# Optimization experiments

Hardware: AMD Instinct MI355X
Metric: run time of the kernel (lower is better)

## Reference

```python
import jax, jax.numpy as jnp
import numpy as np
import math

B, L, S, D = 4, 4096, 4096, 256
EPS = 1e-5

def _layernorm(x, g, b):
    mu = jnp.mean(x, axis=-1, keepdims=True)
    var = jnp.mean(jnp.square(x - mu), axis=-1, keepdims=True)
    return (x - mu) * jax.lax.rsqrt(var + EPS) * g + b

def setup_inputs() -> dict:
    key = jax.random.key(0)
    ks = jax.random.split(key, 14)
    s = 1.0 / math.sqrt(D)
    s2 = 1.0 / math.sqrt(2 * D)
    inp = {
        "source": jax.random.normal(ks[0], (B, L, D), jnp.float32),
        "target": jax.random.normal(ks[1], (B, S, D), jnp.float32),
        # linear weights stored as [in, out]
        "Wq": jax.random.uniform(ks[2], (D, D), jnp.float32, -s, s),
        "bq": jnp.zeros((D,), jnp.float32),
        "Wk": jax.random.uniform(ks[3], (D, D), jnp.float32, -s, s),
        "bk": jnp.zeros((D,), jnp.float32),
        "Wv": jax.random.uniform(ks[4], (D, D), jnp.float32, -s, s),
        "bv": jnp.zeros((D,), jnp.float32),
        "Wm": jax.random.uniform(ks[5], (D, D), jnp.float32, -s, s),
        "bm": jnp.zeros((D,), jnp.float32),
        "g1": jnp.ones((D,), jnp.float32),
        "beta1": jnp.zeros((D,), jnp.float32),
        "W1": jax.random.uniform(ks[6], (2 * D, 2 * D), jnp.float32, -s2, s2),
        "W2": jax.random.uniform(ks[7], (2 * D, D), jnp.float32, -s2, s2),
        "g2": jnp.ones((D,), jnp.float32),
        "beta2": jnp.zeros((D,), jnp.float32),
    }
    return inp

def reference(source, target, Wq, bq, Wk, bk, Wv, bv, Wm, bm, g1, beta1, W1, W2, g2, beta2):
    q = source @ Wq + bq              # [B, L, D]
    k = target @ Wk + bk              # [B, S, D]
    v = target @ Wv + bv              # [B, S, D]
    scale = 1.0 / math.sqrt(D)
    scores = jnp.einsum("bld,bsd->bls", q, k) * scale   # [B, L, S] materialized, as in source
    attn = jax.nn.softmax(scores, axis=-1)
    message = jnp.einsum("bls,bsd->bld", attn, v)        # [B, L, D]
    message = message @ Wm + bm
    message = _layernorm(message, g1, beta1)
    h = jnp.concatenate([source, message], axis=-1)      # [B, L, 2D]
    h = jax.nn.gelu(h @ W1, approximate=False)           # torch GELU is exact erf
    message = _layernorm(h @ W2, g2, beta2)
    return source + message
```

## Files before the change

### kernel.cpp

```cpp
#include <hip/hip_runtime.h>

typedef __bf16 bf16x8 __attribute__((ext_vector_type(8)));
typedef float f32x16 __attribute__((ext_vector_type(16)));
typedef float f32x4 __attribute__((ext_vector_type(4)));
typedef unsigned int u32;
typedef unsigned int u32x4 __attribute__((ext_vector_type(4)));
typedef unsigned short u16;
typedef unsigned short u16x4 __attribute__((ext_vector_type(4)));
typedef unsigned short u16x8 __attribute__((ext_vector_type(8)));

#define DEV static __device__ __forceinline__
#define AS1 __attribute__((address_space(1)))
#define AS3 __attribute__((address_space(3)))

DEV u16 f2bf(float f){
  unsigned u = __float_as_uint(f);
  u += 0x7FFFu + ((u >> 16) & 1u);
  return (u16)(u >> 16);
}
DEV float bf2f(u16 h){ return __uint_as_float(((u32)h) << 16); }

DEV void stage16(const u16* gsrc, const u16* ldst){
  __builtin_amdgcn_global_load_lds((const AS1 u32*)(unsigned long long)gsrc,
                                   (AS3 u32*)(u32)(unsigned long long)ldst,
                                   16, 0, 0);
}

constexpr int BATCH = 4, LQ = 4096, SK = 4096, DH = 256, BL = BATCH * LQ;
constexpr int NHALF = 2;
constexpr int ITERS = SK / NHALF / 64;

__global__ void prep_weights(const float* __restrict__ Wq, const float* __restrict__ Wk,
                             const float* __restrict__ Wv, const float* __restrict__ Wm,
                             const float* __restrict__ W1, const float* __restrict__ W2,
                             const float* __restrict__ bk, const float* __restrict__ bv,
                             u16* __restrict__ WqT, u16* __restrict__ WkvT,
                             u16* __restrict__ WmT,
                             u16* __restrict__ W1T, u16* __restrict__ W2T,
                             float* __restrict__ bkv){
  int idx = blockIdx.x * 256 + threadIdx.x;
  if (idx < 262144){
    int which = idx >> 16, i2 = idx & 65535;
    int r = i2 >> 8, c = i2 & 255;
    const float* S = (which==0)?Wq:(which==1)?Wk:(which==2)?Wv:Wm;
    u16*         D = (which==0)?WqT:(which==1)?WkvT:(which==2)?(WkvT+65536):WmT;
    D[c*256 + r] = f2bf(S[i2]);
  } else if (idx < 524288){
    int i2 = idx - 262144;
    int r = i2 >> 9, c = i2 & 511;
    W1T[c*512 + r] = f2bf(W1[i2]);
  } else if (idx < 655360){
    int i2 = idx - 524288;
    int r = i2 >> 8, c = i2 & 255;
    W2T[(size_t)c*512 + r] = f2bf(W2[i2]);
  } else if (idx < 655872){
    int i2 = idx - 655360;
    bkv[i2] = (i2 < 256) ? bk[i2] : bv[i2 - 256];
  }
}

template<bool A_F32, int EPI, bool WH>
__global__ __launch_bounds__(256, 2) void gemm128(
  const void* __restrict__ Ap, int lda, const u16* __restrict__ BTp,
  const float* __restrict__ bias, void* __restrict__ outp, void* __restrict__ outp2,
  u16* __restrict__ hcat,
  int M, int N, int K, float scale)
{
  __shared__ u16 A_lds[128 * 64];
  __shared__ u16 B_lds[128 * 64];
  const int tid = threadIdx.x, lane = tid & 63, wid = tid >> 6;
  const int ql = lane & 31, g = lane >> 5;
  const int m0 = blockIdx.y * 128, n0 = blockIdx.x * 128;
  const int mr = (wid & 1) * 64, nr = (wid >> 1) * 64;

  f32x16 acc[2][2] = {};
  f32x4 afreg[8];
  u32x4 abreg[4];
  u32x4 breg[4];
  const float* Af = (const float*)Ap;
  const u16*   Ab = (const u16*)Ap;

#define G_LOAD_A(kb) do { \
    if constexpr (A_F32){ \
      _Pragma("unroll") \
      for (int i = 0; i < 8; i++){ int item = tid + i*256; int r = item>>4, c = (item&15)*4; \
        afreg[i] = *(const f32x4*)&Af[(size_t)(m0+r)*lda + (kb)*64 + c]; } \
    } else { \
      _Pragma("unroll") \
      for (int i = 0; i < 4; i++){ int item = tid + i*256; int r = item>>3, c = (item&7)*8; \
        abreg[i] = *(const u32x4*)&Ab[(size_t)(m0+r)*lda + (kb)*64 + c]; } \
    } \
  } while(0)
#define G_LOAD_B(kb) do { \
    _Pragma("unroll") \
    for (int i = 0; i < 4; i++){ int item = tid + i*256; int r = item>>3, c = (item&7)*8; \
      breg[i] = *(const u32x4*)&BTp[(size_t)(n0+r)*K + (kb)*64 + c]; } \
  } while(0)

  G_LOAD_A(0); G_LOAD_B(0);

  const int nkb = K >> 6;
  for (int kb = 0; kb < nkb; ++kb){
    __syncthreads();
    if constexpr (A_F32){
      #pragma unroll
      for (int i = 0; i < 8; i++){ int item = tid + i*256; int r = item>>4, c = (item&15)*4;
        u16x4 h; h[0]=f2bf(afreg[i][0]); h[1]=f2bf(afreg[i][1]);
                 h[2]=f2bf(afreg[i][2]); h[3]=f2bf(afreg[i][3]);
        *(u16x4*)&A_lds[r*64 + (c ^ ((r&7)*8))] = h;
        if constexpr (WH){
          if (n0 == 0) *(u16x4*)&hcat[(size_t)(m0+r)*512 + kb*64 + c] = h;
        }
      }
    } else {
      #pragma unroll
      for (int i = 0; i < 4; i++){ int item = tid + i*256; int r = item>>3, c = (item&7)*8;
        *(u32x4*)&A_lds[r*64 + (c ^ ((r&7)*8))] = abreg[i]; }
    }
    #pragma unroll
    for (int i = 0; i < 4; i++){ int item = tid + i*256; int r = item>>3, c = (item&7)*8;
      *(u32x4*)&B_lds[r*64 + (c ^ ((r&7)*8))] = breg[i]; }
    __syncthreads();
    if (kb + 1 < nkb){ G_LOAD_A(kb+1); G_LOAD_B(kb+1); }

    #pragma unroll
    for (int kk = 0; kk < 4; kk++){
      bf16x8 af[2], bf[2];
      #pragma unroll
      for (int mi = 0; mi < 2; mi++)
        af[mi] = __builtin_bit_cast(bf16x8,
          *(const u32x4*)&A_lds[(mr+mi*32+ql)*64 + ((kk*16+g*8) ^ ((ql&7)*8))]);
      #pragma unroll
      for (int ni = 0; ni < 2; ni++)
        bf[ni] = __builtin_bit_cast(bf16x8,
          *(const u32x4*)&B_lds[(nr+ni*32+ql)*64 + ((kk*16+g*8) ^ ((ql&7)*8))]);
      #pragma unroll
      for (int mi = 0; mi < 2; mi++)
        #pragma unroll
        for (int ni = 0; ni < 2; ni++)
          acc[mi][ni] = __builtin_amdgcn_mfma_f32_32x32x16_bf16(af[mi], bf[ni], acc[mi][ni], 0, 0, 0);
    }
  }

  #pragma unroll
  for (int mi = 0; mi < 2; mi++){
    #pragma unroll
    for (int ni = 0; ni < 2; ni++){
      const int col = n0 + nr + ni*32 + ql;
      const float bv = bias ? bias[col] : 0.f;
      if constexpr (EPI == 4){
        if (col < 256){
          #pragma unroll
          for (int j = 0; j < 16; j++){
            int row = m0 + mr + mi*32 + (j&3) + 8*(j>>2) + 4*g;
            ((u16*)outp)[(size_t)row*256 + col] = f2bf(acc[mi][ni][j] + bv);
          }
        } else {
          const int col2 = col - 256;
          #pragma unroll
          for (int qd = 0; qd < 4; qd++){
            u16x4 h;
            #pragma unroll
            for (int i = 0; i < 4; i++) h[i] = f2bf(acc[mi][ni][qd*4+i] + bv);
            int row0 = m0 + mr + mi*32 + qd*8 + 4*g;
            int bb = row0 >> 12, ss = row0 & 4095;
            *(u16x4*)&((u16*)outp2)[((size_t)bb*DH + col2)*SK + ss] = h;
          }
        }
      } else {
        #pragma unroll
        for (int j = 0; j < 16; j++){
          int row = m0 + mr + mi*32 + (j&3) + 8*(j>>2) + 4*g;
          float v = acc[mi][ni][j] + bv;
          if constexpr (EPI == 0){
            ((u16*)outp)[(size_t)row*N + col] = f2bf(v * scale);
          } else {
            v = 0.5f * v * (1.f + erff(v * 0.70710678118f));
            ((u16*)outp)[(size_t)row*N + col] = f2bf(v);
          }
        }
      }
    }
  }
}

template<int MODE>
__global__ __launch_bounds__(256, 2) void gemm_ln(
  const u16* __restrict__ Ab, const u16* __restrict__ opart,
  const float* __restrict__ stats,
  const u16* __restrict__ BTp, const float* __restrict__ bias,
  const float* __restrict__ gamma, const float* __restrict__ beta,
  const float* __restrict__ src, void* __restrict__ outp, int K)
{
  __shared__ __align__(16) char smem[36864];
  u16* A_lds = (u16*)smem;
  u16* B_lds = (u16*)(smem + 4096);
  float* scratch = (float*)smem;

  const int tid = threadIdx.x, lane = tid & 63, wid = tid >> 6;
  const int ql = lane & 31, g = lane >> 5;
  const int m0 = blockIdx.x * 32;
  const int ar = tid >> 3, ac = (tid & 7) * 8;

  float winv = 0.f;
  if constexpr (MODE == 0){
    int row = m0 + ar;
    winv = 1.f / (stats[row] + stats[(size_t)BL + row]);
  }

  f32x16 acc[2] = {};
  u32x4 areg, areg2;
  u32x4 breg[8];

#define LN_LOAD_A(kb) do { \
    if constexpr (MODE == 0){ \
      areg  = *(const u32x4*)&opart[(size_t)(m0+ar)*DH + (kb)*64 + ac]; \
      areg2 = *(const u32x4*)&opart[(size_t)BL*DH + (size_t)(m0+ar)*DH + (kb)*64 + ac]; \
    } else { \
      areg  = *(const u32x4*)&Ab[(size_t)(m0+ar)*K + (kb)*64 + ac]; \
    } } while(0)
#define LN_LOAD_B(kb) do { \
    _Pragma("unroll") \
    for (int i = 0; i < 8; i++){ int item = tid + i*256; int r = item>>3, c = (item&7)*8; \
      breg[i] = *(const u32x4*)&BTp[(size_t)r*K + (kb)*64 + c]; } \
  } while(0)

  LN_LOAD_A(0); LN_LOAD_B(0);

  const int nkb = K >> 6;
  for (int kb = 0; kb < nkb; ++kb){
    __syncthreads();
    if constexpr (MODE == 0){
      u16x8 h;
      #pragma unroll
      for (int e = 0; e < 8; e++){
        u16 h0 = (u16)(areg[e>>1]  >> ((e&1)*16));
        u16 h1 = (u16)(areg2[e>>1] >> ((e&1)*16));
        h[e] = f2bf((bf2f(h0) + bf2f(h1)) * winv);
      }
      *(u16x8*)&A_lds[ar*64 + (ac ^ ((ar&7)*8))] = h;
    } else {
      *(u32x4*)&A_lds[ar*64 + (ac ^ ((ar&7)*8))] = areg;
    }
    #pragma unroll
    for (int i = 0; i < 8; i++){ int item = tid + i*256; int r = item>>3, c = (item&7)*8;
      *(u32x4*)&B_lds[r*64 + (c ^ ((r&7)*8))] = breg[i]; }
    __syncthreads();
    if (kb + 1 < nkb){ LN_LOAD_A(kb+1); LN_LOAD_B(kb+1); }

    #pragma unroll
    for (int kk = 0; kk < 4; kk++){
      bf16x8 af = __builtin_bit_cast(bf16x8,
        *(const u32x4*)&A_lds[ql*64 + ((kk*16+g*8) ^ ((ql&7)*8))]);
      #pragma unroll
      for (int ni = 0; ni < 2; ni++){
        bf16x8 bf = __builtin_bit_cast(bf16x8,
          *(const u32x4*)&B_lds[(wid*64+ni*32+ql)*64 + ((kk*16+g*8) ^ ((ql&7)*8))]);
        acc[ni] = __builtin_amdgcn_mfma_f32_32x32x16_bf16(af, bf, acc[ni], 0, 0, 0);
      }
    }
  }

  __syncthreads();

  float bv0 = 0.f, bv1 = 0.f;
  if constexpr (MODE == 0){ bv0 = bias[wid*64 + ql]; bv1 = bias[wid*64 + 32 + ql]; }
  #pragma unroll
  for (int ni = 0; ni < 2; ni++)
    #pragma unroll
    for (int j = 0; j < 16; j++){
      int row = (j&3) + 8*(j>>2) + 4*g;
      scratch[row*257 + wid*64 + ni*32 + ql] = acc[ni][j] + (ni ? bv1 : bv0);
    }
  __syncthreads();

  f32x4 gv = *(const f32x4*)&gamma[lane*4];
  f32x4 bvv = *(const f32x4*)&beta[lane*4];
  #pragma unroll
  for (int rr = 0; rr < 8; rr++){
    const int row = wid*8 + rr;
    f32x4 v = *(const f32x4*)&scratch[row*257 + lane*4];
    float s1 = v[0]+v[1]+v[2]+v[3];
    float s2 = v[0]*v[0]+v[1]*v[1]+v[2]*v[2]+v[3]*v[3];
    #pragma unroll
    for (int m = 1; m < 64; m <<= 1){ s1 += __shfl_xor(s1, m, 64); s2 += __shfl_xor(s2, m, 64); }
    float mu = s1 * (1.f/DH);
    float var = s2 * (1.f/DH) - mu*mu;
    float rstd = rsqrtf(var + 1e-5f);
    if constexpr (MODE == 0){
      u16x4 h;
      #pragma unroll
      for (int i = 0; i < 4; i++) h[i] = f2bf((v[i]-mu)*rstd*gv[i] + bvv[i]);
      *(u16x4*)&((u16*)outp)[(size_t)(m0+row)*512 + 256 + lane*4] = h;
    } else {
      f32x4 s = *(const f32x4*)&src[(size_t)(m0+row)*DH + lane*4];
      f32x4 o;
      #pragma unroll
      for (int i = 0; i < 4; i++) o[i] = s[i] + (v[i]-mu)*rstd*gv[i] + bvv[i];
      *(f32x4*)&((float*)outp)[(size_t)(m0+row)*DH + lane*4] = o;
    }
  }
}

__global__ __launch_bounds__(512, 2) void attn_kernel(
  const u16* __restrict__ qb, const u16* __restrict__ kb,
  const u16* __restrict__ vtb, u16* __restrict__ opart, float* __restrict__ stats)
{
  __shared__ u16 K_lds[2][64 * 256];
  __shared__ u16 VT_lds[2][256 * 64];
  __shared__ u32x4 P_exch[4][4][64];
  __shared__ float L_exch[4][2][32];

  const int tid = threadIdx.x;
  const int wid = tid >> 6, lane = tid & 63;
  const int ql = lane & 31, g = lane >> 5;
  const int qpair = wid >> 1, sh = wid & 1;
  const int b = blockIdx.y, half = blockIdx.z;
  const int qrow0 = blockIdx.x * 128 + qpair * 32;
  const int s0base = half * (SK / NHALF);

  const u16* kbase = kb  + (size_t)b * SK * DH;
  const u16* vbase = vtb + (size_t)b * DH * SK;

#define STAGE_K(bi, s0) do { \
    _Pragma("unroll") \
    for (int i = 0; i < 4; i++){ \
      int grp = tid + i*512; int s = grp>>5, slot = grp&31; \
      stage16(kbase + (size_t)((s0)+s)*DH + ((slot ^ (s&31))<<3), \
              &K_lds[bi][(i*512 + wid*64)*8]); \
    } } while(0)
#define STAGE_V(bi, s0) do { \
    _Pragma("unroll") \
    for (int i = 0; i < 4; i++){ \
      int grp = tid + i*512; int d = grp>>3, slot = grp&7; \
      stage16(vbase + (size_t)d*SK + (s0) + ((slot ^ (d&7))<<3), \
              &VT_lds[bi][(i*512 + wid*64)*8]); \
    } } while(0)

  STAGE_K(0, s0base);
  STAGE_V(0, s0base);

  bf16x8 qf[16];
  {
    const u16* qp = qb + ((size_t)(b*LQ + qrow0 + ql)) * DH + g * 8;
    #pragma unroll
    for (int kk = 0; kk < 16; kk++)
      qf[kk] = __builtin_bit_cast(bf16x8, *(const u32x4*)(qp + kk*16));
  }

  f32x16 accO[4] = {};
  float l_lane = 0.f;

  __syncthreads();

  for (int it = 0; it < ITERS; ++it){
    const int cur = it & 1;
    if (it + 1 < ITERS){
      STAGE_K(cur ^ 1, s0base + (it+1)*64);
      STAGE_V(cur ^ 1, s0base + (it+1)*64);
    }

    f32x16 ps = {};
    __builtin_amdgcn_s_setprio(1);
    #pragma unroll
    for (int kk = 0; kk < 16; ++kk){
      bf16x8 kf = __builtin_bit_cast(bf16x8,
        *(const u32x4*)&K_lds[cur][(sh*32+ql)*256 + (((kk*2+g) ^ ql)<<3)]);
      ps = __builtin_amdgcn_mfma_f32_32x32x16_bf16(kf, qf[kk], ps, 0, 0, 0);
    }
    __builtin_amdgcn_s_setprio(0);

    #pragma unroll
    for (int j = 0; j < 16; j++) ps[j] = exp2f(ps[j]);
    float s8[8];
    #pragma unroll
    for (int j = 0; j < 8; j++) s8[j] = ps[j] + ps[j+8];
    l_lane += ((s8[0]+s8[4]) + (s8[1]+s8[5])) + ((s8[2]+s8[6]) + (s8[3]+s8[7]));

    u32 Wp[4][2];
    #pragma unroll
    for (int qd = 0; qd < 4; qd++)
      #pragma unroll
      for (int h = 0; h < 2; h++){
        float lo = ps[qd*4 + 2*h], hi = ps[qd*4 + 2*h + 1];
        asm("v_cvt_pk_bf16_f32 %0, %1, %2" : "=v"(Wp[qd][h]) : "v"(lo), "v"(hi));
      }
    #pragma unroll
    for (int i = 0; i < 2; i++){
      const int qp2 = i * 2;
      u32 a0 = Wp[qp2][0], b0 = Wp[qp2+1][0];
      u32 a1 = Wp[qp2][1], b1 = Wp[qp2+1][1];
      asm("v_permlane32_swap_b32 %0, %1" : "+v"(a0), "+v"(b0));
      asm("v_permlane32_swap_b32 %0, %1" : "+v"(a1), "+v"(b1));
      u32x4 w; w[0] = a0; w[1] = a1; w[2] = b0; w[3] = b1;
      P_exch[qpair][sh*2 + i][lane] = w;
    }

    asm volatile("s_waitcnt lgkmcnt(0)" ::: "memory");
    __builtin_amdgcn_s_barrier();
    __builtin_amdgcn_sched_barrier(0);

    bf16x8 pf0 = __builtin_bit_cast(bf16x8, P_exch[qpair][0][lane]);
    bf16x8 pf1 = __builtin_bit_cast(bf16x8, P_exch[qpair][1][lane]);
    bf16x8 pf2 = __builtin_bit_cast(bf16x8, P_exch[qpair][2][lane]);
    bf16x8 pf3 = __builtin_bit_cast(bf16x8, P_exch[qpair][3][lane]);

    __builtin_amdgcn_s_setprio(1);
    #pragma unroll
    for (int dt = 0; dt < 4; dt++){
      const int dtg = sh*4 + dt;
      bf16x8 vf0 = __builtin_bit_cast(bf16x8,
        *(const u32x4*)&VT_lds[cur][(dtg*32+ql)*64 + (((0*2+g) ^ (ql&7))<<3)]);
      accO[dt] = __builtin_amdgcn_mfma_f32_32x32x16_bf16(vf0, pf0, accO[dt], 0, 0, 0);
      bf16x8 vf1 = __builtin_bit_cast(bf16x8,
        *(const u32x4*)&VT_lds[cur][(dtg*32+ql)*64 + (((1*2+g) ^ (ql&7))<<3)]);
      accO[dt] = __builtin_amdgcn_mfma_f32_32x32x16_bf16(vf1, pf1, accO[dt], 0, 0, 0);
      bf16x8 vf2 = __builtin_bit_cast(bf16x8,
        *(const u32x4*)&VT_lds[cur][(dtg*32+ql)*64 + (((2*2+g) ^ (ql&7))<<3)]);
      accO[dt] = __builtin_amdgcn_mfma_f32_32x32x16_bf16(vf2, pf2, accO[dt], 0, 0, 0);
      bf16x8 vf3 = __builtin_bit_cast(bf16x8,
        *(const u32x4*)&VT_lds[cur][(dtg*32+ql)*64 + (((3*2+g) ^ (ql&7))<<3)]);
      accO[dt] = __builtin_amdgcn_mfma_f32_32x32x16_bf16(vf3, pf3, accO[dt], 0, 0, 0);
    }
    __builtin_amdgcn_s_setprio(0);

    asm volatile("s_waitcnt vmcnt(0) lgkmcnt(0)" ::: "memory");
    __builtin_amdgcn_s_barrier();
    __builtin_amdgcn_sched_barrier(0);
  }

  float l_run = l_lane + __shfl_xor(l_lane, 32, 64);
  if (g == 0) L_exch[qpair][sh][ql] = l_run;
  __syncthreads();
  float l_tot = l_run + L_exch[qpair][sh^1][ql];

  const int rowb = b * LQ + qrow0;
  if (sh == 0 && g == 0)
    stats[(size_t)half*BL + rowb + ql] = l_tot;

  float* scratch = (float*)&K_lds[0][0] + wid * 1056;
  #pragma unroll
  for (int dt = 0; dt < 4; dt++){
    const int dtg = sh*4 + dt;
    #pragma unroll
    for (int j = 0; j < 16; j++){
      int dl = (j&3) + 8*(j>>2) + 4*g;
      scratch[ql*33 + dl] = accO[dt][j];
    }
    int q2 = lane >> 1, dl2 = (lane & 1) * 16;
    u16x8 h0, h1;
    #pragma unroll
    for (int i = 0; i < 8; i++){ h0[i] = f2bf(scratch[q2*33 + dl2 + i]);
                                 h1[i] = f2bf(scratch[q2*33 + dl2 + 8 + i]); }
    u16* op = &opart[((size_t)half*BL + rowb + q2)*DH + dtg*32 + dl2];
    *(u16x8*)op = h0;
    *(u16x8*)(op + 8) = h1;
  }
}

extern "C" void kernel_launch(void* const* d_in, const int* in_sizes, int n_in,
                              void* d_out, int out_size, void* d_ws, size_t ws_size,
                              hipStream_t stream)
{
  const float* source = (const float*)d_in[0];
  const float* target = (const float*)d_in[1];
  const float* Wq = (const float*)d_in[2];  const float* bq = (const float*)d_in[3];
  const float* Wk = (const float*)d_in[4];  const float* bk = (const float*)d_in[5];
  const float* Wv = (const float*)d_in[6];  const float* bv = (const float*)d_in[7];
  const float* Wm = (const float*)d_in[8];  const float* bm = (const float*)d_in[9];
  const float* g1 = (const float*)d_in[10]; const float* be1 = (const float*)d_in[11];
  const float* W1 = (const float*)d_in[12]; const float* W2 = (const float*)d_in[13];
  const float* g2 = (const float*)d_in[14]; const float* be2 = (const float*)d_in[15];

  char* ws = (char*)d_ws;
  u16* WqT  = (u16*)(ws);
  u16* WkvT = (u16*)(ws + (size_t)(1u<<17));
  u16* WmT  = (u16*)(ws + (size_t)3*(1u<<17));
  u16* W1T  = (u16*)(ws + (size_t)4*(1u<<17));
  u16* W2T  = (u16*)(ws + (size_t)8*(1u<<17));
  float* bkv = (float*)(ws + (size_t)10*(1u<<17));
  size_t off = (size_t)10*(1u<<17) + 4096;
  u16* qbuf  = (u16*)(ws + off); off += (size_t)BL*DH*2;
  u16* kbuf  = (u16*)(ws + off); off += (size_t)BL*DH*2;
  u16* vtbuf = (u16*)(ws + off); off += (size_t)BL*DH*2;
  u16* hcat  = (u16*)(ws + off); off += (size_t)BL*512*2;
  u16* hact  = (u16*)(ws + off); off += (size_t)BL*512*2;
  u16* opart = (u16*)(ws + off); off += (size_t)NHALF*BL*DH*2;
  float* stats = (float*)(ws + off); off += (size_t)NHALF*BL*4;

  prep_weights<<<dim3(2562), 256, 0, stream>>>(Wq, Wk, Wv, Wm, W1, W2, bk, bv,
                                               WqT, WkvT, WmT, W1T, W2T, bkv);

  const float qscale = 1.4426950408889634f / 16.0f;
  gemm128<true, 0, true><<<dim3(2, BL/128), 256, 0, stream>>>(
      source, 256, WqT, bq, qbuf, nullptr, hcat, BL, 256, 256, qscale);
  gemm128<true, 4, false><<<dim3(4, BL/128), 256, 0, stream>>>(
      target, 256, WkvT, bkv, kbuf, vtbuf, nullptr, BL, 512, 256, 1.0f);

  attn_kernel<<<dim3(LQ/128, BATCH, NHALF), 512, 0, stream>>>(qbuf, kbuf, vtbuf, opart, stats);

  gemm_ln<0><<<dim3(BL/32), 256, 0, stream>>>(nullptr, opart, stats, WmT, bm,
                                              g1, be1, nullptr, hcat, 256);

  gemm128<false, 3, false><<<dim3(4, BL/128), 256, 0, stream>>>(
      hcat, 512, W1T, nullptr, hact, nullptr, nullptr, BL, 512, 512, 1.0f);
  gemm_ln<1><<<dim3(BL/32), 256, 0, stream>>>(hact, nullptr, nullptr, W2T, nullptr,
                                              g2, be2, source, d_out, 512);
}
```

Baseline: 171.9 us.

## Fuse W1 GEMM, GELU, W2 GEMM and LayerNorm into one MLP kernel

Replaces the separate W1 GEMM-with-GELU launch and the W2 GEMM+LayerNorm launch with a single fused_mlp kernel. Each 32-row block computes its 32x512 GELU activation tile into LDS and feeds it straight into the second GEMM, so the intermediate activation buffer never goes through global memory and one launch is removed. In exchange each block re-streams the full W1 and W2 weights through LDS, uses about 68 KB of shared memory (which may limit occupancy), and has only BL/32 blocks with no double-buffering of weight loads. The generic gemm_ln template is specialised into a Wm-only kernel.

```diff
diff --git a/kernel.cpp b/kernel.cpp
--- a/kernel.cpp
+++ b/kernel.cpp
@@ -171,27 +171,20 @@
         #pragma unroll
         for (int j = 0; j < 16; j++){
           int row = m0 + mr + mi*32 + (j&3) + 8*(j>>2) + 4*g;
-          float v = acc[mi][ni][j] + bv;
-          if constexpr (EPI == 0){
-            ((u16*)outp)[(size_t)row*N + col] = f2bf(v * scale);
-          } else {
-            v = 0.5f * v * (1.f + erff(v * 0.70710678118f));
-            ((u16*)outp)[(size_t)row*N + col] = f2bf(v);
-          }
+          ((u16*)outp)[(size_t)row*N + col] = f2bf((acc[mi][ni][j] + bv) * scale);
         }
       }
     }
   }
 }
 
-template<int MODE>
-__global__ __launch_bounds__(256, 2) void gemm_ln(
-  const u16* __restrict__ Ab, const u16* __restrict__ opart,
-  const float* __restrict__ stats,
+__global__ __launch_bounds__(256, 2) void gemm_ln_wm(
+  const u16* __restrict__ opart, const float* __restrict__ stats,
   const u16* __restrict__ BTp, const float* __restrict__ bias,
   const float* __restrict__ gamma, const float* __restrict__ beta,
-  const float* __restrict__ src, void* __restrict__ outp, int K)
+  u16* __restrict__ outp)
 {
+  constexpr int K = 256;
   __shared__ __align__(16) char smem[36864];
   u16* A_lds = (u16*)smem;
   u16* B_lds = (u16*)(smem + 4096);
@@ -202,51 +195,42 @@
   const int m0 = blockIdx.x * 32;
   const int ar = tid >> 3, ac = (tid & 7) * 8;
 
-  float winv = 0.f;
-  if constexpr (MODE == 0){
-    int row = m0 + ar;
-    winv = 1.f / (stats[row] + stats[(size_t)BL + row]);
-  }
+  float winv;
+  { int row = m0 + ar;
+    winv = 1.f / (stats[row] + stats[(size_t)BL + row]); }
 
   f32x16 acc[2] = {};
   u32x4 areg, areg2;
   u32x4 breg[8];
 
-#define LN_LOAD_A(kb) do { \
-    if constexpr (MODE == 0){ \
-      areg  = *(const u32x4*)&opart[(size_t)(m0+ar)*DH + (kb)*64 + ac]; \
-      areg2 = *(const u32x4*)&opart[(size_t)BL*DH + (size_t)(m0+ar)*DH + (kb)*64 + ac]; \
-    } else { \
-      areg  = *(const u32x4*)&Ab[(size_t)(m0+ar)*K + (kb)*64 + ac]; \
-    } } while(0)
-#define LN_LOAD_B(kb) do { \
+#define WM_LOAD_A(kb) do { \
+    areg  = *(const u32x4*)&opart[(size_t)(m0+ar)*DH + (kb)*64 + ac]; \
+    areg2 = *(const u32x4*)&opart[(size_t)BL*DH + (size_t)(m0+ar)*DH + (kb)*64 + ac]; \
+  } while(0)
+#define WM_LOAD_B(kb) do { \
     _Pragma("unroll") \
     for (int i = 0; i < 8; i++){ int item = tid + i*256; int r = item>>3, c = (item&7)*8; \
       breg[i] = *(const u32x4*)&BTp[(size_t)r*K + (kb)*64 + c]; } \
   } while(0)
 
-  LN_LOAD_A(0); LN_LOAD_B(0);
+  WM_LOAD_A(0); WM_LOAD_B(0);
 
   const int nkb = K >> 6;
   for (int kb = 0; kb < nkb; ++kb){
     __syncthreads();
-    if constexpr (MODE == 0){
-      u16x8 h;
+    { u16x8 h;
       #pragma unroll
       for (int e = 0; e < 8; e++){
         u16 h0 = (u16)(areg[e>>1]  >> ((e&1)*16));
         u16 h1 = (u16)(areg2[e>>1] >> ((e&1)*16));
         h[e] = f2bf((bf2f(h0) + bf2f(h1)) * winv);
       }
-      *(u16x8*)&A_lds[ar*64 + (ac ^ ((ar&7)*8))] = h;
-    } else {
-      *(u32x4*)&A_lds[ar*64 + (ac ^ ((ar&7)*8))] = areg;
-    }
+      *(u16x8*)&A_lds[ar*64 + (ac ^ ((ar&7)*8))] = h; }
     #pragma unroll
     for (int i = 0; i < 8; i++){ int item = tid + i*256; int r = item>>3, c = (item&7)*8;
       *(u32x4*)&B_lds[r*64 + (c ^ ((r&7)*8))] = breg[i]; }
     __syncthreads();
-    if (kb + 1 < nkb){ LN_LOAD_A(kb+1); LN_LOAD_B(kb+1); }
+    if (kb + 1 < nkb){ WM_LOAD_A(kb+1); WM_LOAD_B(kb+1); }
 
     #pragma unroll
     for (int kk = 0; kk < 4; kk++){
@@ -263,8 +247,7 @@
 
   __syncthreads();
 
-  float bv0 = 0.f, bv1 = 0.f;
-  if constexpr (MODE == 0){ bv0 = bias[wid*64 + ql]; bv1 = bias[wid*64 + 32 + ql]; }
+  float bv0 = bias[wid*64 + ql], bv1 = bias[wid*64 + 32 + ql];
   #pragma unroll
   for (int ni = 0; ni < 2; ni++)
     #pragma unroll
@@ -287,18 +270,123 @@
     float mu = s1 * (1.f/DH);
     float var = s2 * (1.f/DH) - mu*mu;
     float rstd = rsqrtf(var + 1e-5f);
-    if constexpr (MODE == 0){
-      u16x4 h;
-      #pragma unroll
-      for (int i = 0; i < 4; i++) h[i] = f2bf((v[i]-mu)*rstd*gv[i] + bvv[i]);
-      *(u16x4*)&((u16*)outp)[(size_t)(m0+row)*512 + 256 + lane*4] = h;
-    } else {
-      f32x4 s = *(const f32x4*)&src[(size_t)(m0+row)*DH + lane*4];
-      f32x4 o;
-      #pragma unroll
-      for (int i = 0; i < 4; i++) o[i] = s[i] + (v[i]-mu)*rstd*gv[i] + bvv[i];
-      *(f32x4*)&((float*)outp)[(size_t)(m0+row)*DH + lane*4] = o;
-    }
+    u16x4 h;
+    #pragma unroll
+    for (int i = 0; i < 4; i++) h[i] = f2bf((v[i]-mu)*rstd*gv[i] + bvv[i]);
+    *(u16x4*)&outp[(size_t)(m0+row)*512 + 256 + lane*4] = h;
+  }
+}
+
+__global__ __launch_bounds__(256, 2) void fused_mlp(
+  const u16* __restrict__ hcat, const u16* __restrict__ W1T,
+  const u16* __restrict__ W2T, const float* __restrict__ gamma,
+  const float* __restrict__ beta, const float* __restrict__ src,
+  float* __restrict__ outp)
+{
+  __shared__ __align__(16) char smem[69632];
+  u16* A1 = (u16*)smem;
+  u16* B1 = (u16*)(smem + 4096);
+  u16* Hl = (u16*)smem;
+  u16* B2 = (u16*)(smem + 36864);
+  float* scratch = (float*)smem;
+
+  const int tid = threadIdx.x, lane = tid & 63, wid = tid >> 6;
+  const int ql = lane & 31, g = lane >> 5;
+  const int m0 = blockIdx.x * 32;
+
+  f32x16 acc1[4] = {};
+  for (int kb = 0; kb < 8; ++kb){
+    if (kb) __syncthreads();
+    { int r = tid >> 3, slot = tid & 7;
+      stage16(&hcat[(size_t)(m0+r)*512 + kb*64 + ((slot ^ (r&7))<<3)],
+              &A1[tid*8]); }
+    #pragma unroll
+    for (int i = 0; i < 16; i++){
+      int grp = tid + i*256; int r = grp>>3, slot = grp&7;
+      stage16(&W1T[(size_t)r*512 + kb*64 + ((slot ^ (r&7))<<3)], &B1[grp*8]);
+    }
+    __syncthreads();
+    #pragma unroll
+    for (int kk = 0; kk < 4; kk++){
+      bf16x8 af = __builtin_bit_cast(bf16x8,
+        *(const u32x4*)&A1[ql*64 + ((kk*16+g*8) ^ ((ql&7)*8))]);
+      #pragma unroll
+      for (int ni = 0; ni < 4; ni++){
+        int rB = wid*128 + ni*32 + ql;
+        bf16x8 bf = __builtin_bit_cast(bf16x8,
+          *(const u32x4*)&B1[rB*64 + ((kk*16+g*8) ^ ((rB&7)*8))]);
+        acc1[ni] = __builtin_amdgcn_mfma_f32_32x32x16_bf16(af, bf, acc1[ni], 0, 0, 0);
+      }
+    }
+  }
+  __syncthreads();
+
+  #pragma unroll
+  for (int ni = 0; ni < 4; ni++){
+    const int col = wid*128 + ni*32 + ql;
+    const int s = col >> 3;
+    #pragma unroll
+    for (int j = 0; j < 16; j++){
+      int row = (j&3) + 8*(j>>2) + 4*g;
+      float v = acc1[ni][j];
+      v = 0.5f * v * (1.f + erff(v * 0.70710678118f));
+      Hl[row*512 + ((s ^ (row&7))<<3) + (col&7)] = f2bf(v);
+    }
+  }
+  __syncthreads();
+
+  f32x16 acc2[2] = {};
+  for (int kb = 0; kb < 8; ++kb){
+    if (kb) __syncthreads();
+    #pragma unroll
+    for (int i = 0; i < 8; i++){
+      int grp = tid + i*256; int r = grp>>3, slot = grp&7;
+      stage16(&W2T[(size_t)r*512 + kb*64 + ((slot ^ (r&7))<<3)], &B2[grp*8]);
+    }
+    __syncthreads();
+    #pragma unroll
+    for (int kk = 0; kk < 4; kk++){
+      int c0 = kb*64 + kk*16 + g*8;
+      bf16x8 af = __builtin_bit_cast(bf16x8,
+        *(const u32x4*)&Hl[ql*512 + (((c0>>3) ^ (ql&7))<<3)]);
+      #pragma unroll
+      for (int ni = 0; ni < 2; ni++){
+        int rB = wid*64 + ni*32 + ql;
+        bf16x8 bf = __builtin_bit_cast(bf16x8,
+          *(const u32x4*)&B2[rB*64 + ((kk*16+g*8) ^ ((rB&7)*8))]);
+        acc2[ni] = __builtin_amdgcn_mfma_f32_32x32x16_bf16(af, bf, acc2[ni], 0, 0, 0);
+      }
+    }
+  }
+  __syncthreads();
+
+  #pragma unroll
+  for (int ni = 0; ni < 2; ni++)
+    #pragma unroll
+    for (int j = 0; j < 16; j++){
+      int row = (j&3) + 8*(j>>2) + 4*g;
+      scratch[row*257 + wid*64 + ni*32 + ql] = acc2[ni][j];
+    }
+  __syncthreads();
+
+  f32x4 gv = *(const f32x4*)&gamma[lane*4];
+  f32x4 bvv = *(const f32x4*)&beta[lane*4];
+  #pragma unroll
+  for (int rr = 0; rr < 8; rr++){
+    const int row = wid*8 + rr;
+    f32x4 v = *(const f32x4*)&scratch[row*257 + lane*4];
+    float s1 = v[0]+v[1]+v[2]+v[3];
+    float s2 = v[0]*v[0]+v[1]*v[1]+v[2]*v[2]+v[3]*v[3];
+    #pragma unroll
+    for (int m = 1; m < 64; m <<= 1){ s1 += __shfl_xor(s1, m, 64); s2 += __shfl_xor(s2, m, 64); }
+    float mu = s1 * (1.f/DH);
+    float var = s2 * (1.f/DH) - mu*mu;
+    float rstd = rsqrtf(var + 1e-5f);
+    f32x4 s = *(const f32x4*)&src[(size_t)(m0+row)*DH + lane*4];
+    f32x4 o;
+    #pragma unroll
+    for (int i = 0; i < 4; i++) o[i] = s[i] + (v[i]-mu)*rstd*gv[i] + bvv[i];
+    *(f32x4*)&outp[(size_t)(m0+row)*DH + lane*4] = o;
   }
 }
 
@@ -484,7 +572,6 @@
   u16* kbuf  = (u16*)(ws + off); off += (size_t)BL*DH*2;
   u16* vtbuf = (u16*)(ws + off); off += (size_t)BL*DH*2;
   u16* hcat  = (u16*)(ws + off); off += (size_t)BL*512*2;
-  u16* hact  = (u16*)(ws + off); off += (size_t)BL*512*2;
   u16* opart = (u16*)(ws + off); off += (size_t)NHALF*BL*DH*2;
   float* stats = (float*)(ws + off); off += (size_t)NHALF*BL*4;
 
@@ -499,11 +586,8 @@
 
   attn_kernel<<<dim3(LQ/128, BATCH, NHALF), 512, 0, stream>>>(qbuf, kbuf, vtbuf, opart, stats);
 
-  gemm_ln<0><<<dim3(BL/32), 256, 0, stream>>>(nullptr, opart, stats, WmT, bm,
-                                              g1, be1, nullptr, hcat, 256);
-
-  gemm128<false, 3, false><<<dim3(4, BL/128), 256, 0, stream>>>(
-      hcat, 512, W1T, nullptr, hact, nullptr, nullptr, BL, 512, 512, 1.0f);
-  gemm_ln<1><<<dim3(BL/32), 256, 0, stream>>>(hact, nullptr, nullptr, W2T, nullptr,
-                                              g2, be2, source, d_out, 512);
-}
+  gemm_ln_wm<<<dim3(BL/32), 256, 0, stream>>>(opart, stats, WmT, bm, g1, be1, hcat);
+
+  fused_mlp<<<dim3(BL/32), 256, 0, stream>>>(hcat, W1T, W2T, g2, be2, source,
+                                             (float*)d_out);
+}
```

New measurement: 162.8 us. 1.06x faster.
